# Kernel tuning notes

Measured on AMD Instinct MI355X. Metric: run time of the kernel, lower is better.

The kernel has to match this reference:

```python
import jax, jax.numpy as jnp
import numpy as np

H, HK, D = 16, 4, 128          # query heads, kv heads, head_dim
HID, INTER = 2048, 8192        # hidden_size, intermediate_size
L, N_UND = 4096, 3072          # total packed len (sum(sample_lens)), num und tokens
SAMPLE_LENS = [2048, 2048]
EPS = 1e-6


def rmsnorm(x, w, eps=EPS):
    v = jnp.mean(jnp.square(x), axis=-1, keepdims=True)
    return x * jax.lax.rsqrt(v + eps) * w


def setup_inputs() -> dict:
    key = jax.random.key(0)
    ks = jax.random.split(key, 12)
    x = jax.random.normal(ks[0], (N_UND, HID), jnp.float32)
    und_idx = jnp.sort(jax.random.permutation(ks[1], L)[:N_UND]).astype(jnp.int64)
    # RoPE tables (source computes RoPE but its attention consumes pre-RoPE tensors)
    pos = jnp.arange(L, dtype=jnp.float32)
    inv_freq = 1.0 / (10000.0 ** (jnp.arange(0, D, 2, dtype=jnp.float32) / D))
    ang = pos[:, None] * inv_freq[None, :]
    cos = jnp.concatenate([jnp.cos(ang), jnp.cos(ang)], axis=-1)
    sin = jnp.concatenate([jnp.sin(ang), jnp.sin(ang)], axis=-1)
    # block-diagonal causal mask over packed sequence (one causal block per sample)
    offs = np.cumsum([0] + SAMPLE_LENS)
    m = np.zeros((L, L), dtype=bool)
    for a, b in zip(offs[:-1], offs[1:]):
        m[a:b, a:b] = np.tril(np.ones((b - a, b - a), dtype=bool))
    mask = jnp.asarray(m)
    w = lambda k, shape: jax.random.normal(k, shape, jnp.float32) * 0.02
    return dict(
        packed_sequence=x, und_idx=und_idx, cos=cos, sin=sin, mask=mask,
        Wq=w(ks[2], (H * D, HID)), bq=w(ks[3], (H * D,)),
        Wk=w(ks[4], (HK * D, HID)), bk=w(ks[5], (HK * D,)),
        Wv=w(ks[6], (HK * D, HID)), bv=w(ks[7], (HK * D,)),
        Wo=w(ks[8], (HID, H * D)),
        q_norm_w=jnp.ones((D,), jnp.float32), k_norm_w=jnp.ones((D,), jnp.float32),
        ln1_w=jnp.ones((HID,), jnp.float32), ln2_w=jnp.ones((HID,), jnp.float32),
        Wg=w(ks[9], (INTER, HID)), Wu=w(ks[10], (INTER, HID)), Wd=w(ks[11], (HID, INTER)),
    )


def reference(packed_sequence, und_idx, cos, sin, mask, Wq, bq, Wk, bk, Wv, bv, Wo,
              q_norm_w, k_norm_w, ln1_w, ln2_w, Wg, Wu, Wd):
    G = H // HK  # num_key_value_groups
    resid = packed_sequence
    x = rmsnorm(packed_sequence, ln1_w)
    # projections on und tokens only, then scatter into zero-initialized packed tensors
    q = (x @ Wq.T + bq).reshape(-1, H, D)
    k = (x @ Wk.T + bk).reshape(-1, HK, D)
    v = (x @ Wv.T + bv).reshape(-1, HK, D)
    Q = jnp.zeros((L, H, D), x.dtype).at[und_idx].set(q)
    K = jnp.zeros((L, HK, D), x.dtype).at[und_idx].set(k)
    V = jnp.zeros((L, HK, D), x.dtype).at[und_idx].set(v)
    # QK RMSNorm (zero rows stay zero, matching scatter-of-normed-und-rows)
    Q = rmsnorm(Q, q_norm_w)
    K = rmsnorm(K, k_norm_w)
    # NOTE: the source applies apply_rotary_pos_emb(Q, K, cos, sin) but both attention
    # branches consume the pre-RoPE normed tensors, so RoPE has no effect; we mirror that.
    Kx = jnp.repeat(K, G, axis=1)  # [L, H, D] GQA expand (each kv head repeated G times)
    Vx = jnp.repeat(V, G, axis=1)
    scores = jnp.einsum('qhd,khd->hqk', Q, Kx) / jnp.sqrt(jnp.asarray(D, x.dtype))
    scores = jnp.where(mask[None], scores, jnp.finfo(scores.dtype).min)
    attn = jax.nn.softmax(scores, axis=-1)
    ctx = jnp.einsum('hqk,khd->qhd', attn, Vx).reshape(L, H * D)
    attn_out = ctx[und_idx] @ Wo.T
    h = resid + attn_out
    y = rmsnorm(h, ln2_w)
    mlp = (jax.nn.silu(y @ Wg.T) * (y @ Wu.T)) @ Wd.T
    return h + mlp
```

## Files before the change

### kernel.cpp

```cpp
#include <hip/hip_runtime.h>
#include <math.h>


#define NU     3072
#define LPACK  4096
#define HIDN   2048
#define QKV_LD 3072
#define EPSF   1e-6f

typedef unsigned short u16;
typedef unsigned int   u32;
typedef unsigned long long u64;
typedef __attribute__((ext_vector_type(8)))  __bf16 bf16x8;
typedef __attribute__((ext_vector_type(4)))  float  f32x4;
typedef __attribute__((ext_vector_type(16))) float  f32x16;

union FRAG { uint4 q; u16 u[8]; bf16x8 b; };

__device__ __forceinline__ u16 f2bf(float f) {
    u32 u = __float_as_uint(f);
    u32 r = (u + 0x7fffu + ((u >> 16) & 1u)) >> 16;
    return (u16)r;
}
__device__ __forceinline__ float bf2f(u16 h) {
    return __uint_as_float(((u32)h) << 16);
}
__device__ __forceinline__ void gload_lds16(const u16* g, u16* lds) {
    __builtin_amdgcn_global_load_lds(
        (const __attribute__((address_space(1))) u32*)g,
        (__attribute__((address_space(3))) u32*)lds, 16, 0, 0);
}


__global__ __launch_bounds__(256) void inv_init_kernel(int* __restrict__ inv) {
    inv[blockIdx.x * 256 + threadIdx.x] = -1;
}
__global__ __launch_bounds__(256) void inv_set_kernel(const int* __restrict__ und,
                                                      int* __restrict__ inv) {
    int i = blockIdx.x * 256 + threadIdx.x;
    inv[und[i]] = i;
}


struct CvtArgs {
    const float* src[7];
    u16*         dst[7];
    int          n8[7];
};

__global__ __launch_bounds__(256) void cvt_all_kernel(CvtArgs a) {
    int seg = blockIdx.y;
    const float* in = a.src[seg];
    u16* out = a.dst[seg];
    int n8 = a.n8[seg];
    int idx = blockIdx.x * 256 + threadIdx.x;
    int stride = gridDim.x * 256;
    for (int i = idx; i < n8; i += stride) {
        float4 va = *(const float4*)(in + (size_t)i * 8);
        float4 vb = *(const float4*)(in + (size_t)i * 8 + 4);
        FRAG f;
        f.u[0] = f2bf(va.x); f.u[1] = f2bf(va.y); f.u[2] = f2bf(va.z); f.u[3] = f2bf(va.w);
        f.u[4] = f2bf(vb.x); f.u[5] = f2bf(vb.y); f.u[6] = f2bf(vb.z); f.u[7] = f2bf(vb.w);
        *(uint4*)(out + (size_t)i * 8) = f.q;
    }
}


__global__ __launch_bounds__(256) void rmsnorm_bf16_kernel(const float* __restrict__ in,
                                                           const float* __restrict__ w,
                                                           u16* __restrict__ out) {
    int row = blockIdx.x;
    const float4* p = (const float4*)(in + (size_t)row * HIDN);
    float4 a = p[threadIdx.x * 2];
    float4 b = p[threadIdx.x * 2 + 1];
    float ss = a.x*a.x + a.y*a.y + a.z*a.z + a.w*a.w
             + b.x*b.x + b.y*b.y + b.z*b.z + b.w*b.w;
    #pragma unroll
    for (int off = 32; off > 0; off >>= 1) ss += __shfl_xor(ss, off, 64);
    __shared__ float red[4];
    if ((threadIdx.x & 63) == 0) red[threadIdx.x >> 6] = ss;
    __syncthreads();
    float tot = red[0] + red[1] + red[2] + red[3];
    float sc  = rsqrtf(tot * (1.0f / HIDN) + EPSF);
    const float4* wp = (const float4*)w;
    float4 w0 = wp[threadIdx.x * 2], w1 = wp[threadIdx.x * 2 + 1];
    FRAG f;
    f.u[0] = f2bf(a.x*sc*w0.x); f.u[1] = f2bf(a.y*sc*w0.y);
    f.u[2] = f2bf(a.z*sc*w0.z); f.u[3] = f2bf(a.w*sc*w0.w);
    f.u[4] = f2bf(b.x*sc*w1.x); f.u[5] = f2bf(b.y*sc*w1.y);
    f.u[6] = f2bf(b.z*sc*w1.z); f.u[7] = f2bf(b.w*sc*w1.w);
    *(uint4*)(out + (size_t)row * HIDN + threadIdx.x * 8) = f.q;
}


__global__ __launch_bounds__(64) void qnorm_kernel(u16* __restrict__ qkv,
                                                   const float* __restrict__ w) {
    int i = blockIdx.x, h = blockIdx.y, t = threadIdx.x;
    u16* p = qkv + (size_t)i * QKV_LD + h * 128 + t * 2;
    u32 pr = *(u32*)p;
    float x0 = bf2f((u16)(pr & 0xffff)), x1 = bf2f((u16)(pr >> 16));
    float ss = x0*x0 + x1*x1;
    #pragma unroll
    for (int off = 32; off > 0; off >>= 1) ss += __shfl_xor(ss, off, 64);
    float sc = rsqrtf(ss * (1.0f / 128.f) + EPSF);
    float2 wv = *(const float2*)(w + t * 2);
    u32 res = (u32)f2bf(x0*sc*wv.x) | ((u32)f2bf(x1*sc*wv.y) << 16);
    *(u32*)p = res;
}


__global__ __launch_bounds__(64) void scatter_kv_kernel(const u16* __restrict__ qkvb,
                                                        const int* __restrict__ inv,
                                                        const float* __restrict__ knw,
                                                        u16* __restrict__ Kb,
                                                        u16* __restrict__ Vb) {
    int l = blockIdx.x, hkk = blockIdx.y, t = threadIdx.x;
    int i = inv[l];
    size_t off = (size_t)l * 512 + hkk * 128 + t * 2;
    if (i < 0) {
        *(u32*)(Kb + off) = 0u;
        *(u32*)(Vb + off) = 0u;
        return;
    }
    const u16* kp = qkvb + (size_t)i * QKV_LD + 2048 + hkk * 128 + t * 2;
    u32 kv = *(const u32*)kp;
    float k0 = bf2f((u16)(kv & 0xffff)), k1 = bf2f((u16)(kv >> 16));
    float ss = k0*k0 + k1*k1;
    #pragma unroll
    for (int off2 = 32; off2 > 0; off2 >>= 1) ss += __shfl_xor(ss, off2, 64);
    float sc = rsqrtf(ss * (1.0f / 128.f) + EPSF);
    float2 wv = *(const float2*)(knw + t * 2);
    u32 res = (u32)f2bf(k0*sc*wv.x) | ((u32)f2bf(k1*sc*wv.y) << 16);
    *(u32*)(Kb + off) = res;
    const u16* vp = qkvb + (size_t)i * QKV_LD + 2560 + hkk * 128 + t * 2;
    *(u32*)(Vb + off) = *(const u32*)vp;
}


template <int MODE>
__global__ __launch_bounds__(256, 2) void gemm_bf16_kernel(
        const u16* __restrict__ A, int lda,
        const u16* __restrict__ B0, const u16* __restrict__ B1, const u16* __restrict__ B2,
        int n1, int n2, int ldb,
        const float* __restrict__ bias0, const float* __restrict__ bias1,
        const float* __restrict__ bias2,
        const float* __restrict__ addend,
        void* __restrict__ Cout, int ldc, int K)
{
    __shared__ u16 As[128 * 64];
    __shared__ u16 Bs[128 * 64];
    const int tid = threadIdx.x;
    const int w = tid >> 6, lane = tid & 63;
    const int gx = gridDim.x;
    int id = blockIdx.y * gx + blockIdx.x;
    const int cpx = (gridDim.x * gridDim.y) >> 3;
    id = (id & 7) * cpx + (id >> 3);
    const int m0 = (id / gx) * 128, n0 = (id % gx) * 128;
    const u16* Bp; const float* bias; int nb;
    if (n0 < n1)      { Bp = B0; bias = bias0; nb = n0; }
    else if (n0 < n2) { Bp = B1; bias = bias1; nb = n0 - n1; }
    else              { Bp = B2; bias = bias2; nb = n0 - n2; }
    const int wr = w >> 1, wc = w & 1;
    const int cl = lane & 15, kg = lane >> 4;

    f32x4 acc[4][4];
    #pragma unroll
    for (int i = 0; i < 4; ++i)
        #pragma unroll
        for (int j = 0; j < 4; ++j)
            #pragma unroll
            for (int r = 0; r < 4; ++r) acc[i][j][r] = 0.f;

    for (int k0 = 0; k0 < K; k0 += 64) {
        #pragma unroll
        for (int j = 0; j < 4; ++j) {
            int slot = j * 256 + tid;
            int row = slot >> 3, jp = slot & 7;
            int j2 = jp ^ (row & 7);
            gload_lds16(A + (size_t)(m0 + row) * lda + k0 + j2 * 8,
                        &As[(j * 256 + w * 64) * 8]);
        }
        #pragma unroll
        for (int j = 0; j < 4; ++j) {
            int slot = j * 256 + tid;
            int row = slot >> 3, jp = slot & 7;
            int j2 = jp ^ (row & 7);
            gload_lds16(Bp + (size_t)(nb + row) * ldb + k0 + j2 * 8,
                        &Bs[(j * 256 + w * 64) * 8]);
        }
        __syncthreads();
        #pragma unroll
        for (int ks = 0; ks < 2; ++ks) {
            FRAG af[4], bfr[4];
            #pragma unroll
            for (int mi = 0; mi < 4; ++mi) {
                int row = wr * 64 + mi * 16 + cl;
                int dblk = ks * 4 + kg;
                af[mi].q = *(const uint4*)&As[row * 64 + ((dblk ^ (row & 7)) * 8)];
            }
            #pragma unroll
            for (int ni = 0; ni < 4; ++ni) {
                int row = wc * 64 + ni * 16 + cl;
                int dblk = ks * 4 + kg;
                bfr[ni].q = *(const uint4*)&Bs[row * 64 + ((dblk ^ (row & 7)) * 8)];
            }
            #pragma unroll
            for (int mi = 0; mi < 4; ++mi)
                #pragma unroll
                for (int ni = 0; ni < 4; ++ni)
                    acc[mi][ni] = __builtin_amdgcn_mfma_f32_16x16x32_bf16(
                        af[mi].b, bfr[ni].b, acc[mi][ni], 0, 0, 0);
        }
        __syncthreads();
    }
    #pragma unroll
    for (int mi = 0; mi < 4; ++mi) {
        #pragma unroll
        for (int ni = 0; ni < 4; ++ni) {
            int gcol = n0 + wc * 64 + ni * 16 + cl;
            float bv = 0.f;
            if (MODE == 0) bv = bias[nb + wc * 64 + ni * 16 + cl];
            #pragma unroll
            for (int r = 0; r < 4; ++r) {
                int grow = m0 + wr * 64 + mi * 16 + kg * 4 + r;
                float v = acc[mi][ni][r] + bv;
                if (MODE == 0) {
                    ((u16*)Cout)[(size_t)grow * ldc + gcol] = f2bf(v);
                } else {
                    v += addend[(size_t)grow * ldc + gcol];
                    ((float*)Cout)[(size_t)grow * ldc + gcol] = v;
                }
            }
        }
    }
}


__global__ __launch_bounds__(256, 2) void gemm_gateup_bf16_kernel(
        const u16* __restrict__ A,
        const u16* __restrict__ Bg, const u16* __restrict__ Bu,
        u16* __restrict__ act, int ldc)
{
    __shared__ u16 As[128 * 64];
    __shared__ u16 Gs[128 * 64];
    __shared__ u16 Us[128 * 64];
    const int tid = threadIdx.x;
    const int w = tid >> 6, lane = tid & 63;
    const int gx = gridDim.x;
    int id = blockIdx.y * gx + blockIdx.x;
    const int cpx = (gridDim.x * gridDim.y) >> 3;
    id = (id & 7) * cpx + (id >> 3);
    const int m0 = (id / gx) * 128, n0 = (id % gx) * 128;
    const int wr = w >> 1, wc = w & 1;
    const int cl = lane & 15, kg = lane >> 4;

    f32x4 ag[4][4], au[4][4];
    #pragma unroll
    for (int i = 0; i < 4; ++i)
        #pragma unroll
        for (int j = 0; j < 4; ++j)
            #pragma unroll
            for (int r = 0; r < 4; ++r) { ag[i][j][r] = 0.f; au[i][j][r] = 0.f; }

    for (int k0 = 0; k0 < HIDN; k0 += 64) {
        #pragma unroll
        for (int j = 0; j < 4; ++j) {
            int slot = j * 256 + tid;
            int row = slot >> 3, jp = slot & 7;
            int j2 = jp ^ (row & 7);
            gload_lds16(A + (size_t)(m0 + row) * HIDN + k0 + j2 * 8,
                        &As[(j * 256 + w * 64) * 8]);
            gload_lds16(Bg + (size_t)(n0 + row) * HIDN + k0 + j2 * 8,
                        &Gs[(j * 256 + w * 64) * 8]);
            gload_lds16(Bu + (size_t)(n0 + row) * HIDN + k0 + j2 * 8,
                        &Us[(j * 256 + w * 64) * 8]);
        }
        __syncthreads();
        #pragma unroll
        for (int ks = 0; ks < 2; ++ks) {
            FRAG af[4], gf[4], uf[4];
            #pragma unroll
            for (int mi = 0; mi < 4; ++mi) {
                int row = wr * 64 + mi * 16 + cl;
                int dblk = ks * 4 + kg;
                af[mi].q = *(const uint4*)&As[row * 64 + ((dblk ^ (row & 7)) * 8)];
            }
            #pragma unroll
            for (int ni = 0; ni < 4; ++ni) {
                int row = wc * 64 + ni * 16 + cl;
                int dblk = ks * 4 + kg;
                gf[ni].q = *(const uint4*)&Gs[row * 64 + ((dblk ^ (row & 7)) * 8)];
                uf[ni].q = *(const uint4*)&Us[row * 64 + ((dblk ^ (row & 7)) * 8)];
            }
            #pragma unroll
            for (int mi = 0; mi < 4; ++mi)
                #pragma unroll
                for (int ni = 0; ni < 4; ++ni) {
                    ag[mi][ni] = __builtin_amdgcn_mfma_f32_16x16x32_bf16(
                        af[mi].b, gf[ni].b, ag[mi][ni], 0, 0, 0);
                    au[mi][ni] = __builtin_amdgcn_mfma_f32_16x16x32_bf16(
                        af[mi].b, uf[ni].b, au[mi][ni], 0, 0, 0);
                }
        }
        __syncthreads();
    }
    #pragma unroll
    for (int mi = 0; mi < 4; ++mi) {
        #pragma unroll
        for (int ni = 0; ni < 4; ++ni) {
            int gcol = n0 + wc * 64 + ni * 16 + cl;
            #pragma unroll
            for (int r = 0; r < 4; ++r) {
                int grow = m0 + wr * 64 + mi * 16 + kg * 4 + r;
                float g = ag[mi][ni][r], u = au[mi][ni][r];
                float s = g / (1.f + __expf(-g));
                act[(size_t)grow * ldc + gcol] = f2bf(s * u);
            }
        }
    }
}


__global__ __launch_bounds__(256, 2) void attn_mfma_kernel(
        const u16* __restrict__ qkv,
        const u16* __restrict__ Kb,
        const u16* __restrict__ Vb,
        const int* __restrict__ und,
        u16* __restrict__ ctxb)
{
    int id = blockIdx.y * 24 + blockIdx.x;
    id = (id & 7) * 48 + (id >> 3);
    const int h = id / 24, hk = h >> 2;
    const int i0 = (id % 24) * 128;
    const int tid = threadIdx.x;
    const int w = tid >> 6, lane = tid & 63;
    const int ql = lane & 31, hi = lane >> 5;

    __shared__ __align__(16) unsigned char SM[36864];
    u16*  Kt = (u16*)SM;
    u16*  Vt = (u16*)(SM + 16384);
    float* Ot = (float*)SM;

    const int iq  = i0 + w * 32 + ql;
    const int pqv = und[iq];
    const int rsv = pqv & ~2047;
    const int kend_w = __shfl(pqv, 31, 64);
    const int kbeg_w = __shfl(pqv, 0, 64) & ~2047;
    const int kbeg_b = und[i0] & ~2047;
    const int kend_b = und[i0 + 127];
    const int nt = ((kend_b - kbeg_b) >> 5) + 1;

    FRAG qf[8];
    const u16* qbase = qkv + (size_t)iq * QKV_LD + h * 128;
    #pragma unroll
    for (int ds = 0; ds < 8; ++ds)
        qf[ds].q = *(const uint4*)(qbase + ds * 16 + hi * 8);

    f32x16 Oa[4];
    #pragma unroll
    for (int dg = 0; dg < 4; ++dg)
        #pragma unroll
        for (int r = 0; r < 16; ++r) Oa[dg][r] = 0.f;
    float m_run = -1e30f, l_run = 0.f;
    const float SCALE = 0.08838834764831845f;

    const int r2 = tid >> 4, c = tid & 15;

    FRAG vr0, vr1;
    {
        #pragma unroll
        for (int j = 0; j < 2; ++j) {
            int sb = (j * 4 + w) * 64;
            int slot = sb + lane;
            int r = slot >> 4, jp = slot & 15;
            int jj = jp ^ (r & 15);
            gload_lds16(Kb + (size_t)(kbeg_b + r) * 512 + hk * 128 + jj * 8,
                        &Kt[sb * 8]);
        }
        const u16* v0 = Vb + (size_t)(kbeg_b + 2 * r2) * 512 + hk * 128 + c * 8;
        vr0.q = *(const uint4*)v0;
        vr1.q = *(const uint4*)(v0 + 512);
    }

    for (int t = 0; t < nt; ++t) {
        const int cur = t & 1;
        const int k0 = kbeg_b + t * 32;
        #pragma unroll
        for (int i = 0; i < 8; ++i) {
            u32 val = (u32)vr0.u[i] | ((u32)vr1.u[i] << 16);
            *(u32*)&Vt[cur * 4608 + (c * 8 + i) * 36 + r2 * 2] = val;
        }
        __syncthreads();
        if (t + 1 < nt) {
            int kn = k0 + 32;
            #pragma unroll
            for (int j = 0; j < 2; ++j) {
                int sb = (j * 4 + w) * 64;
                int slot = sb + lane;
                int r = slot >> 4, jp = slot & 15;
                int jj = jp ^ (r & 15);
                gload_lds16(Kb + (size_t)(kn + r) * 512 + hk * 128 + jj * 8,
                            &Kt[(cur ^ 1) * 4096 + sb * 8]);
            }
            const u16* v0 = Vb + (size_t)(kn + 2 * r2) * 512 + hk * 128 + c * 8;
            vr0.q = *(const uint4*)v0;
            vr1.q = *(const uint4*)(v0 + 512);
        }
        if (k0 + 31 >= kbeg_w && k0 <= kend_w) {
            f32x16 st;
            #pragma unroll
            for (int r = 0; r < 16; ++r) st[r] = 0.f;
            __builtin_amdgcn_s_setprio(1);
            #pragma unroll
            for (int ds = 0; ds < 8; ++ds) {
                FRAG kf;
                kf.q = *(const uint4*)&Kt[cur * 4096 + ql * 128 +
                                          (((ds * 2 + hi) ^ (ql & 15)) * 8)];
                st = __builtin_amdgcn_mfma_f32_32x32x16_bf16(kf.b, qf[ds].b, st, 0, 0, 0);
            }
            __builtin_amdgcn_s_setprio(0);
            int kh4 = k0 + (hi << 2);
            #pragma unroll
            for (int r = 0; r < 16; ++r) {
                int key = kh4 + (r & 3) + ((r >> 2) << 3);
                st[r] = (key >= rsv && key <= pqv) ? st[r] * SCALE : -1e30f;
            }
            float ma = fmaxf(fmaxf(st[0], st[1]), fmaxf(st[2], st[3]));
            float mb = fmaxf(fmaxf(st[4], st[5]), fmaxf(st[6], st[7]));
            float mc = fmaxf(fmaxf(st[8], st[9]), fmaxf(st[10], st[11]));
            float md = fmaxf(fmaxf(st[12], st[13]), fmaxf(st[14], st[15]));
            float mloc = fmaxf(fmaxf(ma, mb), fmaxf(mc, md));
            float mfull = fmaxf(mloc, __shfl_xor(mloc, 32, 64));
            float mnew = fmaxf(m_run, mfull);
            float corr = __expf(m_run - mnew);
            #pragma unroll
            for (int r = 0; r < 16; ++r)
                st[r] = (st[r] > -1e29f) ? __expf(st[r] - mnew) : 0.f;
            float sa = (st[0] + st[1]) + (st[2] + st[3]);
            float sb2 = (st[4] + st[5]) + (st[6] + st[7]);
            float sc2 = (st[8] + st[9]) + (st[10] + st[11]);
            float sd = (st[12] + st[13]) + (st[14] + st[15]);
            float psum = (sa + sb2) + (sc2 + sd);
            psum += __shfl_xor(psum, 32, 64);
            l_run = l_run * corr + psum;
            if (__any(mnew > m_run)) {
                #pragma unroll
                for (int r = 0; r < 16; ++r) {
                    float cr = __shfl(corr, (r & 3) + ((r >> 2) << 3) + (hi << 2), 64);
                    #pragma unroll
                    for (int dg = 0; dg < 4; ++dg) Oa[dg][r] *= cr;
                }
            }
            m_run = mnew;
            u32 pa[2][4];
            #pragma unroll
            for (int s = 0; s < 2; ++s) {
                #pragma unroll
                for (int t2 = 0; t2 < 2; ++t2) {
                    u32 a, b;
                    asm volatile("v_cvt_pk_bf16_f32 %0, %1, %2"
                                 : "=v"(a) : "v"(st[8*s + 2*t2]), "v"(st[8*s + 2*t2 + 1]));
                    asm volatile("v_cvt_pk_bf16_f32 %0, %1, %2"
                                 : "=v"(b) : "v"(st[8*s + 4 + 2*t2]), "v"(st[8*s + 4 + 2*t2 + 1]));
                    asm volatile("v_permlane32_swap_b32 %0, %1" : "+v"(a), "+v"(b));
                    pa[s][t2] = a; pa[s][t2 + 2] = b;
                }
            }
            __builtin_amdgcn_s_setprio(1);
            #pragma unroll
            for (int s = 0; s < 2; ++s) {
                FRAG pau;
                pau.q = make_uint4(pa[s][0], pa[s][1], pa[s][2], pa[s][3]);
                #pragma unroll
                for (int dg = 0; dg < 4; ++dg) {
                    FRAG vfr;
                    const u16* vp = &Vt[cur * 4608 + (dg * 32 + ql) * 36 +
                                        s * 16 + hi * 8];
                    *(u64*)&vfr.u[0] = *(const u64*)vp;
                    *(u64*)&vfr.u[4] = *(const u64*)(vp + 4);
                    Oa[dg] = __builtin_amdgcn_mfma_f32_32x32x16_bf16(
                        pau.b, vfr.b, Oa[dg], 0, 0, 0);
                }
            }
            __builtin_amdgcn_s_setprio(0);
        }
    }
    __syncthreads();

    float linv = 1.f / l_run;
    #pragma unroll
    for (int dg = 0; dg < 4; ++dg) {
        #pragma unroll
        for (int r = 0; r < 16; ++r)
            Ot[w * 1152 + ((r & 3) + ((r >> 2) << 3) + (hi << 2)) * 36 + ql] = Oa[dg][r];
        __syncthreads();
        float4 v0 = *(const float4*)&Ot[w * 1152 + ql * 36 + hi * 16 + 0];
        float4 v1 = *(const float4*)&Ot[w * 1152 + ql * 36 + hi * 16 + 4];
        float4 v2 = *(const float4*)&Ot[w * 1152 + ql * 36 + hi * 16 + 8];
        float4 v3 = *(const float4*)&Ot[w * 1152 + ql * 36 + hi * 16 + 12];
        FRAG a, b;
        a.u[0] = f2bf(v0.x * linv); a.u[1] = f2bf(v0.y * linv);
        a.u[2] = f2bf(v0.z * linv); a.u[3] = f2bf(v0.w * linv);
        a.u[4] = f2bf(v1.x * linv); a.u[5] = f2bf(v1.y * linv);
        a.u[6] = f2bf(v1.z * linv); a.u[7] = f2bf(v1.w * linv);
        b.u[0] = f2bf(v2.x * linv); b.u[1] = f2bf(v2.y * linv);
        b.u[2] = f2bf(v2.z * linv); b.u[3] = f2bf(v2.w * linv);
        b.u[4] = f2bf(v3.x * linv); b.u[5] = f2bf(v3.y * linv);
        b.u[6] = f2bf(v3.z * linv); b.u[7] = f2bf(v3.w * linv);
        u16* dst = ctxb + (size_t)(i0 + w * 32 + ql) * HIDN + h * 128 + dg * 32 + hi * 16;
        *(uint4*)dst = a.q;
        *(uint4*)(dst + 8) = b.q;
        __syncthreads();
    }
}


extern "C" void kernel_launch(void* const* d_in, const int* in_sizes, int n_in,
                              void* d_out, int out_size, void* d_ws, size_t ws_size,
                              hipStream_t stream) {
    const float* x    = (const float*)d_in[0];
    const int*   und  = (const int*)d_in[1];
    const float* Wq  = (const float*)d_in[5];
    const float* bq  = (const float*)d_in[6];
    const float* Wk  = (const float*)d_in[7];
    const float* bk  = (const float*)d_in[8];
    const float* Wv  = (const float*)d_in[9];
    const float* bv  = (const float*)d_in[10];
    const float* Wo  = (const float*)d_in[11];
    const float* qnw = (const float*)d_in[12];
    const float* knw = (const float*)d_in[13];
    const float* ln1 = (const float*)d_in[14];
    const float* ln2 = (const float*)d_in[15];
    const float* Wg  = (const float*)d_in[16];
    const float* Wu  = (const float*)d_in[17];
    const float* Wd  = (const float*)d_in[18];
    float* out = (float*)d_out;

    char* W = (char*)d_ws;
    u16* WqB = (u16*)(W + 0);
    u16* WkB = (u16*)(W + 8388608);
    u16* WvB = (u16*)(W + 10485760);
    u16* WoB = (u16*)(W + 12582912);
    u16* WgB = (u16*)(W + 20971520);
    u16* WuB = (u16*)(W + 54525952);
    u16* WdB = (u16*)(W + 88080384);
    char* R1 = W + 121634816;
    u16* qkvb = (u16*)R1;
    u16* ctxb = (u16*)(R1 + 18874368);
    u16* acth = (u16*)R1;
    float* hbuf = (float*)(W + 153092096);
    u16* xnb = (u16*)(W + 178257920);
    u16* Kbf = xnb;
    u16* Vbf = (u16*)(W + 178257920 + 4194304);
    u16* ynb = xnb;
    int* inv = (int*)(W + 190840832);

    const int BIG = 1 << 30;

    inv_init_kernel<<<16, 256, 0, stream>>>(inv);
    inv_set_kernel<<<12, 256, 0, stream>>>(und, inv);

    CvtArgs ca;
    ca.src[0] = Wq; ca.dst[0] = WqB; ca.n8[0] = 524288;
    ca.src[1] = Wk; ca.dst[1] = WkB; ca.n8[1] = 131072;
    ca.src[2] = Wv; ca.dst[2] = WvB; ca.n8[2] = 131072;
    ca.src[3] = Wo; ca.dst[3] = WoB; ca.n8[3] = 524288;
    ca.src[4] = Wg; ca.dst[4] = WgB; ca.n8[4] = 2097152;
    ca.src[5] = Wu; ca.dst[5] = WuB; ca.n8[5] = 2097152;
    ca.src[6] = Wd; ca.dst[6] = WdB; ca.n8[6] = 2097152;
    cvt_all_kernel<<<dim3(1024, 7), 256, 0, stream>>>(ca);

    rmsnorm_bf16_kernel<<<NU, 256, 0, stream>>>(x, ln1, xnb);
    gemm_bf16_kernel<0><<<dim3(24, 24), 256, 0, stream>>>(
        xnb, 2048, WqB, WkB, WvB, 2048, 2560, 2048,
        bq, bk, bv, nullptr, qkvb, QKV_LD, 2048);
    qnorm_kernel<<<dim3(NU, 16), 64, 0, stream>>>(qkvb, qnw);
    scatter_kv_kernel<<<dim3(LPACK, 4), 64, 0, stream>>>(qkvb, inv, knw, Kbf, Vbf);
    attn_mfma_kernel<<<dim3(24, 16), 256, 0, stream>>>(qkvb, Kbf, Vbf, und, ctxb);
    gemm_bf16_kernel<1><<<dim3(16, 24), 256, 0, stream>>>(
        ctxb, 2048, WoB, WoB, WoB, BIG, BIG, 2048,
        nullptr, nullptr, nullptr, x, hbuf, 2048, 2048);
    rmsnorm_bf16_kernel<<<NU, 256, 0, stream>>>(hbuf, ln2, ynb);
    gemm_gateup_bf16_kernel<<<dim3(32, 24), 256, 0, stream>>>(
        ynb, WgB, WuB, acth, 4096);
    gemm_bf16_kernel<1><<<dim3(16, 24), 256, 0, stream>>>(
        acth, 4096, WdB, WdB, WdB, BIG, BIG, 8192,
        nullptr, nullptr, nullptr, hbuf, out, 2048, 4096);
    gemm_gateup_bf16_kernel<<<dim3(32, 24), 256, 0, stream>>>(
        ynb, WgB + (size_t)4096 * 2048, WuB + (size_t)4096 * 2048, acth, 4096);
    gemm_bf16_kernel<1><<<dim3(16, 24), 256, 0, stream>>>(
        acth, 4096, WdB + 4096, WdB, WdB, BIG, BIG, 8192,
        nullptr, nullptr, nullptr, out, out, 2048, 4096);
}
```

Baseline: 704.3 us.

## Double-buffer LDS tiles in bf16 GEMM and gate/up GEMM kernels

Both GEMM kernels now use ping-pong shared-memory buffers, prefetching the next K tile with async global-to-LDS loads while MFMAs run on the current one. The gate/up kernel halves its K-tile to 32 so the doubled buffers fit in LDS, and changes the swizzle to match. The aim is to hide global load latency behind compute. In exchange, LDS use goes up, which may lower occupancy, and the gate/up kernel takes twice as many loop iterations. The shown hunks drop the leading __syncthreads, so correctness relies on the trailing barrier and the load wait inside the loop.

```diff
diff --git a/kernel.cpp b/kernel.cpp
--- a/kernel.cpp
+++ b/kernel.cpp
@@ -147,8 +147,8 @@
         const float* __restrict__ addend,
         void* __restrict__ Cout, int ldc, int K)
 {
-    __shared__ u16 As[128 * 64];
-    __shared__ u16 Bs[128 * 64];
+    __shared__ u16 As[2][128 * 64];
+    __shared__ u16 Bs[2][128 * 64];
     const int tid = threadIdx.x;
     const int w = tid >> 6, lane = tid & 63;
     const int gx = gridDim.x;
@@ -171,24 +171,34 @@
             #pragma unroll
             for (int r = 0; r < 4; ++r) acc[i][j][r] = 0.f;
 
-    for (int k0 = 0; k0 < K; k0 += 64) {
-        #pragma unroll
-        for (int j = 0; j < 4; ++j) {
-            int slot = j * 256 + tid;
-            int row = slot >> 3, jp = slot & 7;
-            int j2 = jp ^ (row & 7);
-            gload_lds16(A + (size_t)(m0 + row) * lda + k0 + j2 * 8,
-                        &As[(j * 256 + w * 64) * 8]);
-        }
-        #pragma unroll
-        for (int j = 0; j < 4; ++j) {
-            int slot = j * 256 + tid;
-            int row = slot >> 3, jp = slot & 7;
-            int j2 = jp ^ (row & 7);
-            gload_lds16(Bp + (size_t)(nb + row) * ldb + k0 + j2 * 8,
-                        &Bs[(j * 256 + w * 64) * 8]);
-        }
-        __syncthreads();
+    const int NT = K >> 6;
+    #pragma unroll
+    for (int j = 0; j < 4; ++j) {
+        int slot = j * 256 + tid;
+        int row = slot >> 3, jp = slot & 7;
+        int j2 = jp ^ (row & 7);
+        gload_lds16(A + (size_t)(m0 + row) * lda + j2 * 8,
+                    &As[0][(j * 256 + w * 64) * 8]);
+        gload_lds16(Bp + (size_t)(nb + row) * ldb + j2 * 8,
+                    &Bs[0][(j * 256 + w * 64) * 8]);
+    }
+    __syncthreads();
+
+    for (int t = 0; t < NT; ++t) {
+        const int cur = t & 1;
+        if (t + 1 < NT) {
+            int k0 = (t + 1) << 6;
+            #pragma unroll
+            for (int j = 0; j < 4; ++j) {
+                int slot = j * 256 + tid;
+                int row = slot >> 3, jp = slot & 7;
+                int j2 = jp ^ (row & 7);
+                gload_lds16(A + (size_t)(m0 + row) * lda + k0 + j2 * 8,
+                            &As[cur ^ 1][(j * 256 + w * 64) * 8]);
+                gload_lds16(Bp + (size_t)(nb + row) * ldb + k0 + j2 * 8,
+                            &Bs[cur ^ 1][(j * 256 + w * 64) * 8]);
+            }
+        }
         #pragma unroll
         for (int ks = 0; ks < 2; ++ks) {
             FRAG af[4], bfr[4];
@@ -196,13 +206,13 @@
             for (int mi = 0; mi < 4; ++mi) {
                 int row = wr * 64 + mi * 16 + cl;
                 int dblk = ks * 4 + kg;
-                af[mi].q = *(const uint4*)&As[row * 64 + ((dblk ^ (row & 7)) * 8)];
+                af[mi].q = *(const uint4*)&As[cur][row * 64 + ((dblk ^ (row & 7)) * 8)];
             }
             #pragma unroll
             for (int ni = 0; ni < 4; ++ni) {
                 int row = wc * 64 + ni * 16 + cl;
                 int dblk = ks * 4 + kg;
-                bfr[ni].q = *(const uint4*)&Bs[row * 64 + ((dblk ^ (row & 7)) * 8)];
+                bfr[ni].q = *(const uint4*)&Bs[cur][row * 64 + ((dblk ^ (row & 7)) * 8)];
             }
             #pragma unroll
             for (int mi = 0; mi < 4; ++mi)
@@ -241,9 +251,9 @@
         const u16* __restrict__ Bg, const u16* __restrict__ Bu,
         u16* __restrict__ act, int ldc)
 {
-    __shared__ u16 As[128 * 64];
-    __shared__ u16 Gs[128 * 64];
-    __shared__ u16 Us[128 * 64];
+    __shared__ u16 As[2][128 * 32];
+    __shared__ u16 Gs[2][128 * 32];
+    __shared__ u16 Us[2][128 * 32];
     const int tid = threadIdx.x;
     const int w = tid >> 6, lane = tid & 63;
     const int gx = gridDim.x;
@@ -262,35 +272,50 @@
             #pragma unroll
             for (int r = 0; r < 4; ++r) { ag[i][j][r] = 0.f; au[i][j][r] = 0.f; }
 
-    for (int k0 = 0; k0 < HIDN; k0 += 64) {
-        #pragma unroll
-        for (int j = 0; j < 4; ++j) {
-            int slot = j * 256 + tid;
-            int row = slot >> 3, jp = slot & 7;
-            int j2 = jp ^ (row & 7);
-            gload_lds16(A + (size_t)(m0 + row) * HIDN + k0 + j2 * 8,
-                        &As[(j * 256 + w * 64) * 8]);
-            gload_lds16(Bg + (size_t)(n0 + row) * HIDN + k0 + j2 * 8,
-                        &Gs[(j * 256 + w * 64) * 8]);
-            gload_lds16(Bu + (size_t)(n0 + row) * HIDN + k0 + j2 * 8,
-                        &Us[(j * 256 + w * 64) * 8]);
-        }
-        __syncthreads();
-        #pragma unroll
-        for (int ks = 0; ks < 2; ++ks) {
+    const int NT = HIDN >> 5;
+    #pragma unroll
+    for (int j = 0; j < 2; ++j) {
+        int slot = j * 256 + tid;
+        int row = slot >> 2, jp = slot & 3;
+        int j2 = jp ^ (row & 3);
+        gload_lds16(A + (size_t)(m0 + row) * HIDN + j2 * 8,
+                    &As[0][(j * 256 + w * 64) * 8]);
+        gload_lds16(Bg + (size_t)(n0 + row) * HIDN + j2 * 8,
+                    &Gs[0][(j * 256 + w * 64) * 8]);
+        gload_lds16(Bu + (size_t)(n0 + row) * HIDN + j2 * 8,
+                    &Us[0][(j * 256 + w * 64) * 8]);
+    }
+    __syncthreads();
+
+    for (int t = 0; t < NT; ++t) {
+        const int cur = t & 1;
+        if (t + 1 < NT) {
+            int k0 = (t + 1) << 5;
+            #pragma unroll
+            for (int j = 0; j < 2; ++j) {
+                int slot = j * 256 + tid;
+                int row = slot >> 2, jp = slot & 3;
+                int j2 = jp ^ (row & 3);
+                gload_lds16(A + (size_t)(m0 + row) * HIDN + k0 + j2 * 8,
+                            &As[cur ^ 1][(j * 256 + w * 64) * 8]);
+                gload_lds16(Bg + (size_t)(n0 + row) * HIDN + k0 + j2 * 8,
+                            &Gs[cur ^ 1][(j * 256 + w * 64) * 8]);
+                gload_lds16(Bu + (size_t)(n0 + row) * HIDN + k0 + j2 * 8,
+                            &Us[cur ^ 1][(j * 256 + w * 64) * 8]);
+            }
+        }
+        {
             FRAG af[4], gf[4], uf[4];
             #pragma unroll
             for (int mi = 0; mi < 4; ++mi) {
                 int row = wr * 64 + mi * 16 + cl;
-                int dblk = ks * 4 + kg;
-                af[mi].q = *(const uint4*)&As[row * 64 + ((dblk ^ (row & 7)) * 8)];
+                af[mi].q = *(const uint4*)&As[cur][row * 32 + ((kg ^ (row & 3)) * 8)];
             }
             #pragma unroll
             for (int ni = 0; ni < 4; ++ni) {
                 int row = wc * 64 + ni * 16 + cl;
-                int dblk = ks * 4 + kg;
-                gf[ni].q = *(const uint4*)&Gs[row * 64 + ((dblk ^ (row & 7)) * 8)];
-                uf[ni].q = *(const uint4*)&Us[row * 64 + ((dblk ^ (row & 7)) * 8)];
+                gf[ni].q = *(const uint4*)&Gs[cur][row * 32 + ((kg ^ (row & 3)) * 8)];
+                uf[ni].q = *(const uint4*)&Us[cur][row * 32 + ((kg ^ (row & 3)) * 8)];
             }
             #pragma unroll
             for (int mi = 0; mi < 4; ++mi)
```

Measured after the change: 831.7 us. 1.18x slower.
